# Kernel optimization log

Measured on AMD Instinct MI355X. Metric: run time of the kernel, lower is better.

## Reference

```python
import jax, jax.numpy as jnp
import numpy as np

NUM_CLASSES = 9
BASE_SMOOTHING = 0.1
UPWARD_BIAS = 0.2
BATCH = 4_000_000


def setup_inputs() -> dict:
    key = jax.random.key(0)
    k1, k2 = jax.random.split(key)
    logits = jax.random.normal(k1, (BATCH, NUM_CLASSES), dtype=jnp.float32)
    targets = jax.random.randint(k2, (BATCH,), 0, NUM_CLASSES, dtype=jnp.int32)
    return {"logits": logits, "targets": targets}


def _smooth_labels(targets, num_classes):
    # Closed form of the per-sample Python loop in the torch module:
    #   label[t] = 1 - bs - ub  (set, overwriting the base)
    #   label[k] = bs/C + ub * 0.5**(k - t)   for k > t (geometric halving,
    #              including the last class which keeps remaining*0.5)
    #   label[k] = bs/C                        for k < t
    # followed by row normalization.
    base = BASE_SMOOTHING / num_classes
    main = 1.0 - BASE_SMOOTHING - UPWARD_BIAS
    j = jnp.arange(num_classes)  # [C]
    d = j[None, :] - targets[:, None]  # [B, C], class index minus target
    upward = jnp.where(d > 0, UPWARD_BIAS * jnp.exp2(-d.astype(jnp.float32)), 0.0)
    labels = jnp.where(d == 0, main, base + upward)  # [B, C]
    return labels / labels.sum(axis=-1, keepdims=True)


def reference(logits, targets):
    smooth = _smooth_labels(targets, logits.shape[-1])  # [B, C]
    log_probs = jax.nn.log_softmax(logits, axis=-1)      # [B, C]
    loss = -(smooth * log_probs).sum(axis=-1)            # [B]
    return loss.mean()
```

## Files before the change

kernel.cpp:

```cpp
#include <hip/hip_runtime.h>
#include <math.h>

#define NUM_C 9
constexpr float W_BASE = 0.1f / 9.0f;
constexpr float W_MAIN = 0.7f;

constexpr int THREADS = 256;
constexpr int ROWS_PER_BLOCK = 1024;
constexpr int VECS_PER_BLOCK = ROWS_PER_BLOCK * NUM_C / 4;
constexpr int VECS_PER_WAVE = VECS_PER_BLOCK / 4;
constexpr int CALLS_PER_WAVE = VECS_PER_WAVE / 64;

__device__ __forceinline__ void async_copy16(const float4* g, float4* l) {
    __builtin_amdgcn_global_load_lds(
        (const __attribute__((address_space(1))) void*)g,
        (__attribute__((address_space(3))) void*)l,
        16 , 0 , 0 );
}

__global__ __launch_bounds__(THREADS, 4) void ccel_main(
    const float* __restrict__ logits,
    const int* __restrict__ targets,
    float* __restrict__ partials,
    int nRows, int nFullBlocks)
{
    __shared__ float4 lds4[VECS_PER_BLOCK];
    __shared__ float wave_sums[THREADS / 64];

    const int tid = threadIdx.x;
    const int wave = tid >> 6;
    const int lane = tid & 63;
    const long long vecBase = (long long)blockIdx.x * VECS_PER_BLOCK;
    const float4* gv = (const float4*)logits + vecBase;

    if (blockIdx.x < nFullBlocks) {
        const float4* src = gv + wave * VECS_PER_WAVE;
        float4* dst = lds4 + wave * VECS_PER_WAVE;
#pragma unroll
        for (int i = 0; i < CALLS_PER_WAVE; i++) {
            async_copy16(src + i * 64 + lane, dst + i * 64);
        }
    } else {
        const long long totalVecs = ((long long)nRows * NUM_C) / 4;
        for (int i = tid; i < VECS_PER_BLOCK; i += THREADS) {
            if (vecBase + i < totalVecs) lds4[i] = gv[i];
        }
    }
    __syncthreads();

    const int myRow = blockIdx.x * ROWS_PER_BLOCK + tid * 4;
    float acc = 0.0f;

    if (myRow < nRows) {
        const int4 t4 = ((const int4*)targets)[myRow >> 2];
        const int tg[4] = {t4.x, t4.y, t4.z, t4.w};

        float x[36];
        float4* xv = (float4*)x;
#pragma unroll
        for (int i = 0; i < 9; i++) xv[i] = lds4[tid * 9 + i];

#pragma unroll
        for (int k = 0; k < 4; k++) {
            const float* xr = x + k * NUM_C;
            const int t = tg[k];

            float m = xr[0];
#pragma unroll
            for (int j = 1; j < NUM_C; j++) m = fmaxf(m, xr[j]);

            float sum = 0.0f, xt = 0.0f;
#pragma unroll
            for (int j = 0; j < NUM_C; j++) {
                sum += xr[j];
                xt = (t == j) ? xr[j] : xt;
            }

            float g = 0.0f, gt = 0.0f;
#pragma unroll
            for (int j = NUM_C - 1; j >= 1; j--) {
                g = 0.5f * (xr[j] + g);
                gt = (t == j - 1) ? g : gt;
            }

            float es = 0.0f;
#pragma unroll
            for (int j = 0; j < NUM_C; j++) es += __expf(xr[j] - m);
            const float lse = m + __logf(es);

            const float S = 0.98888889f - 0.2f * ldexpf(1.0f, t - 8);
            const float weighted = W_BASE * sum + (W_MAIN - W_BASE) * xt + 0.2f * gt;
            acc += lse - weighted * __builtin_amdgcn_rcpf(S);
        }
    }

#pragma unroll
    for (int off = 32; off > 0; off >>= 1)
        acc += __shfl_down(acc, off, 64);

    if (lane == 0) wave_sums[wave] = acc;
    __syncthreads();
    if (tid == 0) {
        float bsum = 0.0f;
#pragma unroll
        for (int w = 0; w < THREADS / 64; w++) bsum += wave_sums[w];
        partials[blockIdx.x] = bsum;
    }
}

__global__ __launch_bounds__(1024) void ccel_finish(
    const float* __restrict__ partials,
    int n,
    float* __restrict__ out,
    float invBatch)
{
    double acc = 0.0;
    for (int i = threadIdx.x; i < n; i += 1024)
        acc += (double)partials[i];

#pragma unroll
    for (int off = 32; off > 0; off >>= 1)
        acc += __shfl_down(acc, off, 64);

    __shared__ double wsum[16];
    if ((threadIdx.x & 63) == 0) wsum[threadIdx.x >> 6] = acc;
    __syncthreads();
    if (threadIdx.x == 0) {
        double total = 0.0;
#pragma unroll
        for (int w = 0; w < 16; w++) total += wsum[w];
        out[0] = (float)(total * (double)invBatch);
    }
}

extern "C" void kernel_launch(void* const* d_in, const int* in_sizes, int n_in,
                              void* d_out, int out_size, void* d_ws, size_t ws_size,
                              hipStream_t stream) {
    const float* logits = (const float*)d_in[0];
    const int* targets = (const int*)d_in[1];
    const int nRows = in_sizes[1];

    float* partials = (float*)d_ws;
    const int nBlocks = (nRows + ROWS_PER_BLOCK - 1) / ROWS_PER_BLOCK;
    const long long totalVecs = ((long long)nRows * NUM_C) / 4;
    const int nFullBlocks = (int)(totalVecs / VECS_PER_BLOCK);

    ccel_main<<<nBlocks, THREADS, 0, stream>>>(logits, targets, partials,
                                               nRows, nFullBlocks);
    ccel_finish<<<1, 1024, 0, stream>>>(partials, nBlocks, (float*)d_out,
                                        1.0f / (float)nRows);
}
```

Measured before the change: 213.9 us.

## Fuse final reduction into main kernel via last-block atomic counter

```diff
diff --git a/kernel.cpp b/kernel.cpp
--- a/kernel.cpp
+++ b/kernel.cpp
@@ -21,17 +21,24 @@
 __global__ __launch_bounds__(THREADS, 4) void ccel_main(
     const float* __restrict__ logits,
     const int* __restrict__ targets,
+    unsigned* __restrict__ counter,
     float* __restrict__ partials,
-    int nRows, int nFullBlocks)
+    float* __restrict__ out,
+    int nRows, int nFullBlocks, int nBlocks, float invBatch)
 {
     __shared__ float4 lds4[VECS_PER_BLOCK];
     __shared__ float wave_sums[THREADS / 64];
+    __shared__ int is_last;
 
     const int tid = threadIdx.x;
     const int wave = tid >> 6;
     const int lane = tid & 63;
     const long long vecBase = (long long)blockIdx.x * VECS_PER_BLOCK;
     const float4* gv = (const float4*)logits + vecBase;
+
+    const int myRow = blockIdx.x * ROWS_PER_BLOCK + tid * 4;
+    int4 t4 = {0, 0, 0, 0};
+    if (myRow < nRows) t4 = ((const int4*)targets)[myRow >> 2];
 
     if (blockIdx.x < nFullBlocks) {
         const float4* src = gv + wave * VECS_PER_WAVE;
@@ -48,11 +55,9 @@
     }
     __syncthreads();
 
-    const int myRow = blockIdx.x * ROWS_PER_BLOCK + tid * 4;
     float acc = 0.0f;
 
     if (myRow < nRows) {
-        const int4 t4 = ((const int4*)targets)[myRow >> 2];
         const int tg[4] = {t4.x, t4.y, t4.z, t4.w};
 
         float x[36];
@@ -105,31 +110,29 @@
 #pragma unroll
         for (int w = 0; w < THREADS / 64; w++) bsum += wave_sums[w];
         partials[blockIdx.x] = bsum;
+        __threadfence();
+        unsigned old = atomicAdd(counter, 1u);
+        is_last = (old == (unsigned)(nBlocks - 1)) ? 1 : 0;
     }
-}
+    __syncthreads();
 
-__global__ __launch_bounds__(1024) void ccel_finish(
-    const float* __restrict__ partials,
-    int n,
-    float* __restrict__ out,
-    float invBatch)
-{
-    double acc = 0.0;
-    for (int i = threadIdx.x; i < n; i += 1024)
-        acc += (double)partials[i];
-
+    if (is_last) {
+        __threadfence();
+        double dacc = 0.0;
+        for (int i = tid; i < nBlocks; i += THREADS)
+            dacc += (double)partials[i];
 #pragma unroll
-    for (int off = 32; off > 0; off >>= 1)
-        acc += __shfl_down(acc, off, 64);
-
-    __shared__ double wsum[16];
-    if ((threadIdx.x & 63) == 0) wsum[threadIdx.x >> 6] = acc;
-    __syncthreads();
-    if (threadIdx.x == 0) {
-        double total = 0.0;
+        for (int off = 32; off > 0; off >>= 1)
+            dacc += __shfl_down(dacc, off, 64);
+        __shared__ double dsum[THREADS / 64];
+        if (lane == 0) dsum[wave] = dacc;
+        __syncthreads();
+        if (tid == 0) {
+            double total = 0.0;
 #pragma unroll
-        for (int w = 0; w < 16; w++) total += wsum[w];
-        out[0] = (float)(total * (double)invBatch);
+            for (int w = 0; w < THREADS / 64; w++) total += dsum[w];
+            out[0] = (float)(total * (double)invBatch);
+        }
     }
 }
 
@@ -140,13 +143,14 @@
     const int* targets = (const int*)d_in[1];
     const int nRows = in_sizes[1];
 
-    float* partials = (float*)d_ws;
+    unsigned* counter = (unsigned*)d_ws;
+    float* partials = (float*)((char*)d_ws + 16);
     const int nBlocks = (nRows + ROWS_PER_BLOCK - 1) / ROWS_PER_BLOCK;
     const long long totalVecs = ((long long)nRows * NUM_C) / 4;
     const int nFullBlocks = (int)(totalVecs / VECS_PER_BLOCK);
 
-    ccel_main<<<nBlocks, THREADS, 0, stream>>>(logits, targets, partials,
-                                               nRows, nFullBlocks);
-    ccel_finish<<<1, 1024, 0, stream>>>(partials, nBlocks, (float*)d_out,
-                                        1.0f / (float)nRows);
+    hipMemsetAsync(counter, 0, sizeof(unsigned), stream);
+    ccel_main<<<nBlocks, THREADS, 0, stream>>>(logits, targets, counter, partials,
+                                               (float*)d_out, nRows, nFullBlocks,
+                                               nBlocks, 1.0f / (float)nRows);
 }
```

After: 398.0 us. 1.86x slower.

## Replace finish kernel with per-block atomicAdd and prefetch targets before LDS copy

Applied to the files above, without the earlier changes.

```diff
diff --git a/kernel.cpp b/kernel.cpp
--- a/kernel.cpp
+++ b/kernel.cpp
@@ -21,8 +21,8 @@
 __global__ __launch_bounds__(THREADS, 4) void ccel_main(
     const float* __restrict__ logits,
     const int* __restrict__ targets,
-    float* __restrict__ partials,
-    int nRows, int nFullBlocks)
+    float* __restrict__ out,
+    int nRows, int nFullBlocks, float invBatch)
 {
     __shared__ float4 lds4[VECS_PER_BLOCK];
     __shared__ float wave_sums[THREADS / 64];
@@ -32,6 +32,10 @@
     const int lane = tid & 63;
     const long long vecBase = (long long)blockIdx.x * VECS_PER_BLOCK;
     const float4* gv = (const float4*)logits + vecBase;
+
+    const int myRow = blockIdx.x * ROWS_PER_BLOCK + tid * 4;
+    int4 t4 = {0, 0, 0, 0};
+    if (myRow < nRows) t4 = ((const int4*)targets)[myRow >> 2];
 
     if (blockIdx.x < nFullBlocks) {
         const float4* src = gv + wave * VECS_PER_WAVE;
@@ -48,11 +52,9 @@
     }
     __syncthreads();
 
-    const int myRow = blockIdx.x * ROWS_PER_BLOCK + tid * 4;
     float acc = 0.0f;
 
     if (myRow < nRows) {
-        const int4 t4 = ((const int4*)targets)[myRow >> 2];
         const int tg[4] = {t4.x, t4.y, t4.z, t4.w};
 
         float x[36];
@@ -104,32 +106,7 @@
         float bsum = 0.0f;
 #pragma unroll
         for (int w = 0; w < THREADS / 64; w++) bsum += wave_sums[w];
-        partials[blockIdx.x] = bsum;
-    }
-}
-
-__global__ __launch_bounds__(1024) void ccel_finish(
-    const float* __restrict__ partials,
-    int n,
-    float* __restrict__ out,
-    float invBatch)
-{
-    double acc = 0.0;
-    for (int i = threadIdx.x; i < n; i += 1024)
-        acc += (double)partials[i];
-
-#pragma unroll
-    for (int off = 32; off > 0; off >>= 1)
-        acc += __shfl_down(acc, off, 64);
-
-    __shared__ double wsum[16];
-    if ((threadIdx.x & 63) == 0) wsum[threadIdx.x >> 6] = acc;
-    __syncthreads();
-    if (threadIdx.x == 0) {
-        double total = 0.0;
-#pragma unroll
-        for (int w = 0; w < 16; w++) total += wsum[w];
-        out[0] = (float)(total * (double)invBatch);
+        atomicAdd(out, bsum * invBatch);
     }
 }
 
@@ -140,13 +117,12 @@
     const int* targets = (const int*)d_in[1];
     const int nRows = in_sizes[1];
 
-    float* partials = (float*)d_ws;
     const int nBlocks = (nRows + ROWS_PER_BLOCK - 1) / ROWS_PER_BLOCK;
     const long long totalVecs = ((long long)nRows * NUM_C) / 4;
     const int nFullBlocks = (int)(totalVecs / VECS_PER_BLOCK);
 
-    ccel_main<<<nBlocks, THREADS, 0, stream>>>(logits, targets, partials,
-                                               nRows, nFullBlocks);
-    ccel_finish<<<1, 1024, 0, stream>>>(partials, nBlocks, (float*)d_out,
-                                        1.0f / (float)nRows);
+    hipMemsetAsync(d_out, 0, sizeof(float), stream);
+    ccel_main<<<nBlocks, THREADS, 0, stream>>>(logits, targets, (float*)d_out,
+                                               nRows, nFullBlocks,
+                                               1.0f / (float)nRows);
 }
```

Result: slower. 220.4 us (+3.1%).
